# Performance work log

Hardware: AMD Instinct MI355X
Metric: run time of the kernel (lower is better)

The kernel has to match this reference:

```python
import jax, jax.numpy as jnp
import numpy as np

H = 8  # hidden_size

def setup_inputs() -> dict:
    key = jax.random.key(0)
    ks = jax.random.split(key, 7)
    B, T, I = 131072, 48, 5
    s = 1.0 / np.sqrt(H)  # torch LSTM/Linear init scale (uniform bound); use scaled normal
    return {
        "x": jax.random.normal(ks[0], (B, T, I), dtype=jnp.float32),
        "W_ih": jax.random.normal(ks[1], (4 * H, I), dtype=jnp.float32) * s,
        "W_hh": jax.random.normal(ks[2], (4 * H, H), dtype=jnp.float32) * s,
        "b_ih": jax.random.normal(ks[3], (4 * H,), dtype=jnp.float32) * s,
        "b_hh": jax.random.normal(ks[4], (4 * H,), dtype=jnp.float32) * s,
        "fc_W": jax.random.normal(ks[5], (1, H * T), dtype=jnp.float32) * (1.0 / np.sqrt(H * T)),
        "fc_b": jax.random.normal(ks[6], (1,), dtype=jnp.float32) * (1.0 / np.sqrt(H * T)),
    }

def _lstm_forward(x, W_ih, W_hh, b_ih, b_hh):
    # x: [B, T, I]. PyTorch gate order: i, f, g, o.
    B, T, _ = x.shape
    # Precompute input projections for all timesteps: [B, T, 4H] -> [T, B, 4H]
    xp = jnp.einsum('bti,gi->btg', x, W_ih) + b_ih + b_hh
    xp = xp.transpose(1, 0, 2)

    def step(carry, xt):
        h, c = carry
        gates = xt + h @ W_hh.T  # [B, 4H]
        i, f, g, o = jnp.split(gates, 4, axis=-1)
        c = jax.nn.sigmoid(f) * c + jax.nn.sigmoid(i) * jnp.tanh(g)
        h = jax.nn.sigmoid(o) * jnp.tanh(c)
        return (h, c), h

    h0 = jnp.zeros((B, H), dtype=x.dtype)
    c0 = jnp.zeros((B, H), dtype=x.dtype)
    _, hs = jax.lax.scan(step, (h0, c0), xp)  # hs: [T, B, H]
    return hs.transpose(1, 0, 2)  # [B, T, H]

def reference(x, W_ih, W_hh, b_ih, b_hh, fc_W, fc_b):
    B, T, _ = x.shape
    lstm_out = _lstm_forward(x, W_ih, W_hh, b_ih, b_hh)  # [B, T, H]
    preds = lstm_out.reshape(B, T * H) @ fc_W.T + fc_b   # [B, 1]
    return preds.reshape(-1)  # [B]
```

## Files before the change

### kernel.cpp

```cpp
#include <hip/hip_runtime.h>

#define TT 48
#define II 5
#define HID 8

typedef float float2v __attribute__((ext_vector_type(2)));

template<int CTRL>
__device__ __forceinline__ float dppf(float v) {
    return __int_as_float(__builtin_amdgcn_update_dpp(0, __float_as_int(v), CTRL, 0xF, 0xF, true));
}
__device__ __forceinline__ float fexp2(float x){ float r; asm("v_exp_f32 %0, %1":"=v"(r):"v"(x)); return r; }
__device__ __forceinline__ float frcp(float x){ return __builtin_amdgcn_rcpf(x); }

__device__ __forceinline__ float2v pk_lo(float2v acc, float2v w, float2v z) {
    asm("v_pk_fma_f32 %0, %1, %2, %0 op_sel_hi:[0,1,1]" : "+v"(acc) : "v"(w), "v"(z));
    return acc;
}
__device__ __forceinline__ float2v pk_hi(float2v acc, float2v w, float2v z) {
    asm("v_pk_fma_f32 %0, %1, %2, %0 op_sel:[1,0,0] op_sel_hi:[1,1,1]" : "+v"(acc) : "v"(w), "v"(z));
    return acc;
}
__device__ __forceinline__ float2v pk_lo3(float2v w, float2v z, float2v b) {
    float2v d;
    asm("v_pk_fma_f32 %0, %1, %2, %3 op_sel_hi:[0,1,1]" : "=v"(d) : "v"(w), "v"(z), "v"(b));
    return d;
}
__device__ __forceinline__ void pin2(float2v& v) { asm("" : "+v"(v)); }

__global__ __attribute__((amdgpu_flat_work_group_size(64, 64), amdgpu_waves_per_eu(2, 2)))
void lstm_fused(
    const float* __restrict__ x,
    const float* __restrict__ W_ih,
    const float* __restrict__ W_hh,
    const float* __restrict__ b_ih,
    const float* __restrict__ b_hh,
    const float* __restrict__ fc_W,
    const float* __restrict__ fc_b,
    float* __restrict__ out, int B)
{
    __shared__ float s_fc[TT * HID];
    const int tid = threadIdx.x;
    #pragma unroll
    for (int i = tid; i < TT * HID; i += 64) s_fc[i] = fc_W[i];
    __syncthreads();

    const int q    = tid & 7;
    const int slot = tid >> 3;
    const int b0   = (blockIdx.x * 8 + slot) * 2;
    if (b0 >= B) return;

    const float L2E  = 1.44269504088896340736f;
    const float L2E2 = 2.0f * L2E;
    const float sc[4] = {-L2E, -L2E, L2E2, -L2E};

    float2v P[4][7], bias[4];
    #pragma unroll
    for (int g = 0; g < 4; ++g) {
        const int row = g * 8 + q;
        const float s = sc[g];
        P[g][0] = (float2v){s * W_ih[row * II + 0], s * W_ih[row * II + 1]};
        P[g][1] = (float2v){s * W_ih[row * II + 2], s * W_ih[row * II + 3]};
        P[g][2] = (float2v){s * W_ih[row * II + 4], s * W_hh[row * HID + (q ^ 0)]};
        P[g][3] = (float2v){s * W_hh[row * HID + (q ^ 1)], s * W_hh[row * HID + (q ^ 2)]};
        P[g][4] = (float2v){s * W_hh[row * HID + (q ^ 3)], s * W_hh[row * HID + (q ^ 4)]};
        P[g][5] = (float2v){s * W_hh[row * HID + (q ^ 5)], s * W_hh[row * HID + (q ^ 6)]};
        P[g][6] = (float2v){s * W_hh[row * HID + (q ^ 7)], 0.0f};
        const float bb = s * (b_ih[row] + b_hh[row]);
        bias[g] = (float2v){bb, bb};
        #pragma unroll
        for (int j = 0; j < 7; ++j) pin2(P[g][j]);
        pin2(bias[g]);
    }

    const float2* xA = reinterpret_cast<const float2*>(x + (size_t)b0 * (TT * II));
    const float2* xB = reinterpret_cast<const float2*>(x + (size_t)(b0 + 1) * (TT * II));

    float2 curA[5], curB[5], nxtA[5], nxtB[5];
    #pragma unroll
    for (int k = 0; k < 5; ++k) { curA[k] = xA[k]; curB[k] = xB[k]; }

    float hA = 0.f, hB = 0.f, cA = 0.f, cB = 0.f, accA = 0.f, accB = 0.f;

    #pragma unroll 1
    for (int ch = 0; ch < 24; ++ch) {
        if (ch < 23) {
            #pragma unroll
            for (int k = 0; k < 5; ++k) { nxtA[k] = xA[(ch + 1) * 5 + k]; nxtB[k] = xB[(ch + 1) * 5 + k]; }
        }

        #pragma unroll
        for (int s2 = 0; s2 < 2; ++s2) {
            const int t = ch * 2 + s2;

            float2v xs[5];
            #pragma unroll
            for (int i = 0; i < 5; ++i) {
                const int idx = s2 * 5 + i;
                const float a = (idx & 1) ? curA[idx >> 1].y : curA[idx >> 1].x;
                const float b = (idx & 1) ? curB[idx >> 1].y : curB[idx >> 1].x;
                xs[i] = (float2v){a, b};
            }

            const float2v hap0 = (float2v){hA, hB};
            const float2v hap1 = (float2v){dppf<0xB1>(hA), dppf<0xB1>(hB)};
            const float2v hap2 = (float2v){dppf<0x4E>(hA), dppf<0x4E>(hB)};
            const float2v hap3 = (float2v){dppf<0x1B>(hA), dppf<0x1B>(hB)};
            const float2v hap7 = (float2v){dppf<0x141>(hA), dppf<0x141>(hB)};
            const float2v hap6 = (float2v){dppf<0x141>(hap1.x), dppf<0x141>(hap1.y)};
            const float2v hap5 = (float2v){dppf<0x141>(hap2.x), dppf<0x141>(hap2.y)};
            const float2v hap4 = (float2v){dppf<0x141>(hap3.x), dppf<0x141>(hap3.y)};

            float2v gg[4];
            #pragma unroll
            for (int g = 0; g < 4; ++g) {
                float2v a = pk_lo3(P[g][0], xs[0], bias[g]);
                a = pk_hi(a, P[g][0], xs[1]);
                a = pk_lo(a, P[g][1], xs[2]);
                a = pk_hi(a, P[g][1], xs[3]);
                a = pk_lo(a, P[g][2], xs[4]);
                a = pk_hi(a, P[g][2], hap0);
                a = pk_lo(a, P[g][3], hap1);
                a = pk_hi(a, P[g][3], hap2);
                a = pk_lo(a, P[g][4], hap3);
                a = pk_hi(a, P[g][4], hap4);
                a = pk_lo(a, P[g][5], hap5);
                a = pk_hi(a, P[g][5], hap6);
                a = pk_lo(a, P[g][6], hap7);
                gg[g] = a;
            }

            {
                const float Ei = fexp2(gg[0].x), Ef = fexp2(gg[1].x);
                const float Eg = fexp2(gg[2].x), Eo = fexp2(gg[3].x);
                const float sf  = frcp(1.0f + Ef);
                const float rig = frcp((1.0f + Ei) * (1.0f + Eg));
                cA = fmaf(sf, cA, (Eg - 1.0f) * rig);
                const float Ec  = fexp2(cA * L2E2);
                const float roc = frcp((1.0f + Eo) * (1.0f + Ec));
                hA = (Ec - 1.0f) * roc;
            }
            {
                const float Ei = fexp2(gg[0].y), Ef = fexp2(gg[1].y);
                const float Eg = fexp2(gg[2].y), Eo = fexp2(gg[3].y);
                const float sf  = frcp(1.0f + Ef);
                const float rig = frcp((1.0f + Ei) * (1.0f + Eg));
                cB = fmaf(sf, cB, (Eg - 1.0f) * rig);
                const float Ec  = fexp2(cB * L2E2);
                const float roc = frcp((1.0f + Eo) * (1.0f + Ec));
                hB = (Ec - 1.0f) * roc;
            }

            const float fw = s_fc[t * HID + q];
            accA = fmaf(hA, fw, accA);
            accB = fmaf(hB, fw, accB);
        }

        #pragma unroll
        for (int k = 0; k < 5; ++k) { curA[k] = nxtA[k]; curB[k] = nxtB[k]; }
    }

    accA += dppf<0xB1>(accA); accA += dppf<0x4E>(accA); accA += dppf<0x141>(accA);
    accB += dppf<0xB1>(accB); accB += dppf<0x4E>(accB); accB += dppf<0x141>(accB);
    if (q == 0) {
        out[b0] = accA + fc_b[0];
        if (b0 + 1 < B) out[b0 + 1] = accB + fc_b[0];
    }
}

extern "C" void kernel_launch(void* const* d_in, const int* in_sizes, int n_in,
                              void* d_out, int out_size, void* d_ws, size_t ws_size,
                              hipStream_t stream) {
    const float* x    = (const float*)d_in[0];
    const float* W_ih = (const float*)d_in[1];
    const float* W_hh = (const float*)d_in[2];
    const float* b_ih = (const float*)d_in[3];
    const float* b_hh = (const float*)d_in[4];
    const float* fc_W = (const float*)d_in[5];
    const float* fc_b = (const float*)d_in[6];
    float* out = (float*)d_out;

    const int B = in_sizes[0] / (TT * II);
    const int grid = (B + 15) / 16;
    lstm_fused<<<grid, 64, 0, stream>>>(x, W_ih, W_hh, b_ih, b_hh, fc_W, fc_b, out, B);
}
```

Baseline: 107.1 us.

## Use 256-thread blocks, merge sigmoid reciprocals, and make prefetch branchless

Blocks grow from 64 to 256 threads with a waves-per-EU hint of 4 instead of a fixed 2, giving each CU more resident waves to hide the latency of the recurrent chain. The LSTM cell update now folds the forget-gate reciprocal into one shared reciprocal of the product of the three denominators, removing one rcp per element per step. The next-chunk prefetch becomes unconditional and reloads the last chunk on the final iteration. The combined reciprocal risks overflow or precision loss when the exponentials are large, and the higher occupancy target may force register spilling.

Measured after the change: 98.44 us. 1.09x faster.

```diff
diff --git a/kernel.cpp b/kernel.cpp
--- a/kernel.cpp
+++ b/kernel.cpp
@@ -28,7 +28,7 @@
 }
 __device__ __forceinline__ void pin2(float2v& v) { asm("" : "+v"(v)); }
 
-__global__ __attribute__((amdgpu_flat_work_group_size(64, 64), amdgpu_waves_per_eu(2, 2)))
+__global__ __attribute__((amdgpu_flat_work_group_size(256, 256), amdgpu_waves_per_eu(4)))
 void lstm_fused(
     const float* __restrict__ x,
     const float* __restrict__ W_ih,
@@ -41,13 +41,12 @@
 {
     __shared__ float s_fc[TT * HID];
     const int tid = threadIdx.x;
-    #pragma unroll
-    for (int i = tid; i < TT * HID; i += 64) s_fc[i] = fc_W[i];
+    for (int i = tid; i < TT * HID; i += 256) s_fc[i] = fc_W[i];
     __syncthreads();
 
     const int q    = tid & 7;
     const int slot = tid >> 3;
-    const int b0   = (blockIdx.x * 8 + slot) * 2;
+    const int b0   = (blockIdx.x * 32 + slot) * 2;
     if (b0 >= B) return;
 
     const float L2E  = 1.44269504088896340736f;
@@ -84,10 +83,9 @@
 
     #pragma unroll 1
     for (int ch = 0; ch < 24; ++ch) {
-        if (ch < 23) {
-            #pragma unroll
-            for (int k = 0; k < 5; ++k) { nxtA[k] = xA[(ch + 1) * 5 + k]; nxtB[k] = xB[(ch + 1) * 5 + k]; }
-        }
+        const int nc = (ch < 23) ? ch + 1 : 23;
+        #pragma unroll
+        for (int k = 0; k < 5; ++k) { nxtA[k] = xA[nc * 5 + k]; nxtB[k] = xB[nc * 5 + k]; }
 
         #pragma unroll
         for (int s2 = 0; s2 < 2; ++s2) {
@@ -133,22 +131,24 @@
             {
                 const float Ei = fexp2(gg[0].x), Ef = fexp2(gg[1].x);
                 const float Eg = fexp2(gg[2].x), Eo = fexp2(gg[3].x);
-                const float sf  = frcp(1.0f + Ef);
-                const float rig = frcp((1.0f + Ei) * (1.0f + Eg));
-                cA = fmaf(sf, cA, (Eg - 1.0f) * rig);
+                const float Di = 1.f + Ei, Df = 1.f + Ef, Dg = 1.f + Eg;
+                const float Pig = Di * Dg;
+                const float R3  = frcp(Pig * Df);
+                cA = fmaf(Pig, cA, fmaf(Eg, Df, -Df)) * R3;
                 const float Ec  = fexp2(cA * L2E2);
-                const float roc = frcp((1.0f + Eo) * (1.0f + Ec));
-                hA = (Ec - 1.0f) * roc;
+                const float Ro  = frcp((1.f + Eo) * (1.f + Ec));
+                hA = fmaf(Ec, Ro, -Ro);
             }
             {
                 const float Ei = fexp2(gg[0].y), Ef = fexp2(gg[1].y);
                 const float Eg = fexp2(gg[2].y), Eo = fexp2(gg[3].y);
-                const float sf  = frcp(1.0f + Ef);
-                const float rig = frcp((1.0f + Ei) * (1.0f + Eg));
-                cB = fmaf(sf, cB, (Eg - 1.0f) * rig);
+                const float Di = 1.f + Ei, Df = 1.f + Ef, Dg = 1.f + Eg;
+                const float Pig = Di * Dg;
+                const float R3  = frcp(Pig * Df);
+                cB = fmaf(Pig, cB, fmaf(Eg, Df, -Df)) * R3;
                 const float Ec  = fexp2(cB * L2E2);
-                const float roc = frcp((1.0f + Eo) * (1.0f + Ec));
-                hB = (Ec - 1.0f) * roc;
+                const float Ro  = frcp((1.f + Eo) * (1.f + Ec));
+                hB = fmaf(Ec, Ro, -Ro);
             }
 
             const float fw = s_fc[t * HID + q];
@@ -181,6 +181,6 @@
     float* out = (float*)d_out;
 
     const int B = in_sizes[0] / (TT * II);
-    const int grid = (B + 15) / 16;
-    lstm_fused<<<grid, 64, 0, stream>>>(x, W_ih, W_hh, b_ih, b_hh, fc_W, fc_b, out, B);
+    const int grid = (B + 63) / 64;
+    lstm_fused<<<grid, 256, 0, stream>>>(x, W_ih, W_hh, b_ih, b_hh, fc_W, fc_b, out, B);
 }
```
